# Performance work log

Hardware: AMD Instinct MI355X
Metric: run time of the kernel (lower is better)

The kernel has to match this reference:

```python
import jax, jax.numpy as jnp
import numpy as np

EMBEDDING = 1024
PARAMETERS = 4096

def setup_inputs() -> dict:
    key = jax.random.key(0)
    kx, kK, kV = jax.random.split(key, 3)
    x = jax.random.normal(kx, (4, 2048, EMBEDDING), dtype=jnp.float32)
    K = jax.random.normal(kK, (PARAMETERS, EMBEDDING), dtype=jnp.float32)
    V = jax.random.normal(kV, (PARAMETERS, EMBEDDING), dtype=jnp.float32)
    return {"x": x, "K": K, "V": V}

def reference(x, K, V):
    # scores: [b, s, p] = scale * x @ K.T
    scale = EMBEDDING ** (-0.5)
    scores = scale * jnp.einsum('bse,pe->bsp', x, K)
    attn = jax.nn.softmax(scores, axis=-1)
    # out: [b, s, e] = attn @ V
    return jnp.einsum('bsp,pe->bse', attn, V)
```

## Files before the change

### kernel.cpp

```cpp
#include <hip/hip_runtime.h>
#include <hip/hip_bf16.h>

typedef __bf16 bf16x8 __attribute__((ext_vector_type(8)));
typedef __bf16 bf16x4 __attribute__((ext_vector_type(4)));
typedef float floatx4 __attribute__((ext_vector_type(4)));

typedef __attribute__((address_space(1))) const void gas_void;
typedef __attribute__((address_space(3))) void las_void;

__device__ inline void async_load16(const void* g, void* l) {
  __builtin_amdgcn_global_load_lds((gas_void*)g, (las_void*)l, 16, 0, 0);
}

__global__ __launch_bounds__(256) void f32_to_bf16_kernel(const float* __restrict__ in,
                                                          __bf16* __restrict__ out, int n4) {
  int i = blockIdx.x * 256 + threadIdx.x;
  if (i < n4) {
    float4 v = ((const float4*)in)[i];
    bf16x4 o = {(__bf16)v.x, (__bf16)v.y, (__bf16)v.z, (__bf16)v.w};
    ((bf16x4*)out)[i] = o;
  }
}

__global__ __launch_bounds__(256) void transpose_convert_kernel(const float* __restrict__ V,
                                                                __bf16* __restrict__ Vt) {
  __shared__ float tile[64][65];
  const int bx = blockIdx.x;
  const int by = blockIdx.y;
  for (int i = threadIdx.x; i < 64 * 64; i += 256) {
    const int r = i >> 6, c = i & 63;
    tile[r][c] = V[(size_t)(bx * 64 + r) * 1024 + by * 64 + c];
  }
  __syncthreads();
  for (int i = threadIdx.x; i < 64 * 64; i += 256) {
    const int r = i >> 6, c = i & 63;
    Vt[(size_t)(by * 64 + r) * 4096 + bx * 64 + c] = (__bf16)tile[c][r];
  }
}

template <int MODE, int KS, int NS>
__global__ __launch_bounds__(256) void gemm_kernel(const __bf16* __restrict__ A,
                                                   const __bf16* __restrict__ B,
                                                   __bf16* __restrict__ Cb,
                                                   float* __restrict__ Cf,
                                                   float* __restrict__ lsum) {
  constexpr int BK = 32;
  __shared__ __bf16 As[128 * BK];
  __shared__ __bf16 Bs[128 * BK];
  const int t = threadIdx.x;
  const int lane = t & 63;
  const int w = t >> 6;
  const int wr = w >> 1, wc = w & 1;

  const int id = blockIdx.x;
  const int g = id & 7;
  const int s = id >> 3;
  const int mt = g * 8 + (s & 7);
  const int nt = s >> 3;
  const int m0 = mt * 128;
  const int n0 = nt * 128;

  const __bf16* Ab = A + (size_t)m0 * KS;
  const __bf16* Bb = B + (size_t)n0 * KS;

  floatx4 acc[4][4] = {};

  const int f0 = t * 16;
  const int row0 = f0 >> 6;
  const int ke0 = (f0 & 63) >> 1;
  const int f1 = 4096 + t * 16;
  const int row1 = f1 >> 6;
  const int ke1 = (f1 & 63) >> 1;

  for (int k0 = 0; k0 < KS; k0 += BK) {
    async_load16(Ab + (size_t)row0 * KS + k0 + ke0, (char*)As + f0);
    async_load16(Ab + (size_t)row1 * KS + k0 + ke1, (char*)As + f1);
    async_load16(Bb + (size_t)row0 * KS + k0 + ke0, (char*)Bs + f0);
    async_load16(Bb + (size_t)row1 * KS + k0 + ke1, (char*)Bs + f1);
    __builtin_amdgcn_s_waitcnt(0);
    __syncthreads();

    bf16x8 aF[4], bF[4];
    const int krd = (lane >> 4) * 16;
#pragma unroll
    for (int i = 0; i < 4; ++i) {
      const int mr = wr * 64 + i * 16 + (lane & 15);
      aF[i] = *(const bf16x8*)((const char*)As + mr * 64 + krd);
    }
#pragma unroll
    for (int j = 0; j < 4; ++j) {
      const int nr = wc * 64 + j * 16 + (lane & 15);
      bF[j] = *(const bf16x8*)((const char*)Bs + nr * 64 + krd);
    }
#pragma unroll
    for (int i = 0; i < 4; ++i)
#pragma unroll
      for (int j = 0; j < 4; ++j)
        acc[i][j] = __builtin_amdgcn_mfma_f32_16x16x32_bf16(aF[i], bF[j], acc[i][j], 0, 0, 0);
    __syncthreads();
  }

  const int cm = wr * 64 + ((lane >> 4) << 2);
  const int cn = wc * 64 + (lane & 15);
  if (MODE == 0) {
#pragma unroll
    for (int i = 0; i < 4; ++i)
#pragma unroll
      for (int r = 0; r < 4; ++r) {
        const int m = m0 + cm + i * 16 + r;
        float rs = 0.f;
#pragma unroll
        for (int j = 0; j < 4; ++j) {
          const float e = __expf(fminf(acc[i][j][r] * 0.03125f, 30.0f));
          rs += e;
          Cb[(size_t)m * NS + n0 + cn + j * 16] = (__bf16)e;
        }
        rs += __shfl_xor(rs, 1, 64);
        rs += __shfl_xor(rs, 2, 64);
        rs += __shfl_xor(rs, 4, 64);
        rs += __shfl_xor(rs, 8, 64);
        if ((lane & 15) == 0) atomicAdd(&lsum[m], rs);
      }
  } else {
#pragma unroll
    for (int i = 0; i < 4; ++i)
#pragma unroll
      for (int r = 0; r < 4; ++r) {
        const int m = m0 + cm + i * 16 + r;
        const float inv = 1.0f / lsum[m];
#pragma unroll
        for (int j = 0; j < 4; ++j)
          Cf[(size_t)m * NS + n0 + cn + j * 16] = acc[i][j][r] * inv;
      }
  }
}

extern "C" void kernel_launch(void* const* d_in, const int* in_sizes, int n_in,
                              void* d_out, int out_size, void* d_ws, size_t ws_size,
                              hipStream_t stream) {
  const float* x = (const float*)d_in[0];
  const float* K = (const float*)d_in[1];
  const float* V = (const float*)d_in[2];
  float* out = (float*)d_out;

  char* ws = (char*)d_ws;
  __bf16* xb = (__bf16*)ws;
  __bf16* Kb = (__bf16*)(ws + (16u << 20));
  __bf16* Vt = (__bf16*)(ws + (24u << 20));
  __bf16* P  = (__bf16*)(ws + (32u << 20));
  float*  l  = (float*)(ws + (96u << 20));

  f32_to_bf16_kernel<<<8192, 256, 0, stream>>>(x, xb, 8192 * 1024 / 4);
  f32_to_bf16_kernel<<<4096, 256, 0, stream>>>(K, Kb, 4096 * 1024 / 4);
  transpose_convert_kernel<<<dim3(64, 16), 256, 0, stream>>>(V, Vt);
  hipMemsetAsync(l, 0, 8192 * sizeof(float), stream);
  gemm_kernel<0, 1024, 4096><<<2048, 256, 0, stream>>>(xb, Kb, P, nullptr, l);
  gemm_kernel<1, 4096, 1024><<<512, 256, 0, stream>>>(P, Vt, nullptr, out, l);
}
```

Before: 282.5 us.

## Fuse preprocessing kernels and double GEMM K-tile with XOR-swizzled LDS layout

Result: faster. 267.7 us (-5.2%).

```diff
diff --git a/kernel.cpp b/kernel.cpp
--- a/kernel.cpp
+++ b/kernel.cpp
@@ -12,29 +12,46 @@
   __builtin_amdgcn_global_load_lds((gas_void*)g, (las_void*)l, 16, 0, 0);
 }
 
-__global__ __launch_bounds__(256) void f32_to_bf16_kernel(const float* __restrict__ in,
-                                                          __bf16* __restrict__ out, int n4) {
-  int i = blockIdx.x * 256 + threadIdx.x;
-  if (i < n4) {
-    float4 v = ((const float4*)in)[i];
-    bf16x4 o = {(__bf16)v.x, (__bf16)v.y, (__bf16)v.z, (__bf16)v.w};
-    ((bf16x4*)out)[i] = o;
-  }
-}
-
-__global__ __launch_bounds__(256) void transpose_convert_kernel(const float* __restrict__ V,
-                                                                __bf16* __restrict__ Vt) {
-  __shared__ float tile[64][65];
-  const int bx = blockIdx.x;
-  const int by = blockIdx.y;
-  for (int i = threadIdx.x; i < 64 * 64; i += 256) {
-    const int r = i >> 6, c = i & 63;
-    tile[r][c] = V[(size_t)(bx * 64 + r) * 1024 + by * 64 + c];
-  }
-  __syncthreads();
-  for (int i = threadIdx.x; i < 64 * 64; i += 256) {
-    const int r = i >> 6, c = i & 63;
-    Vt[(size_t)(by * 64 + r) * 4096 + bx * 64 + c] = (__bf16)tile[c][r];
+__global__ __launch_bounds__(256) void preprocess_kernel(
+    const float* __restrict__ x, const float* __restrict__ Kp,
+    const float* __restrict__ V, __bf16* __restrict__ xb,
+    __bf16* __restrict__ Kb, __bf16* __restrict__ Vt,
+    float* __restrict__ lsum) {
+  const int b = blockIdx.x;
+  const int t = threadIdx.x;
+  if (b < 2048) {
+#pragma unroll
+    for (int k = 0; k < 4; ++k) {
+      const int i = b * 1024 + k * 256 + t;
+      float4 v = ((const float4*)x)[i];
+      bf16x4 o = {(__bf16)v.x, (__bf16)v.y, (__bf16)v.z, (__bf16)v.w};
+      ((bf16x4*)xb)[i] = o;
+    }
+  } else if (b < 3072) {
+#pragma unroll
+    for (int k = 0; k < 4; ++k) {
+      const int i = (b - 2048) * 1024 + k * 256 + t;
+      float4 v = ((const float4*)Kp)[i];
+      bf16x4 o = {(__bf16)v.x, (__bf16)v.y, (__bf16)v.z, (__bf16)v.w};
+      ((bf16x4*)Kb)[i] = o;
+    }
+  } else if (b < 4096) {
+    __shared__ float tile[64][65];
+    const int bb = b - 3072;
+    const int bx = bb & 63, by = bb >> 6;
+    for (int i = t; i < 64 * 64; i += 256) {
+      const int r = i >> 6, c = i & 63;
+      tile[r][c] = V[(size_t)(bx * 64 + r) * 1024 + by * 64 + c];
+    }
+    __syncthreads();
+    for (int i = t; i < 64 * 64; i += 256) {
+      const int r = i >> 6, c = i & 63;
+      Vt[(size_t)(by * 64 + r) * 4096 + bx * 64 + c] = (__bf16)tile[c][r];
+    }
+  } else {
+#pragma unroll
+    for (int k = 0; k < 8; ++k)
+      ((floatx4*)lsum)[k * 256 + t] = floatx4{0.f, 0.f, 0.f, 0.f};
   }
 }
 
@@ -44,7 +61,7 @@
                                                    __bf16* __restrict__ Cb,
                                                    float* __restrict__ Cf,
                                                    float* __restrict__ lsum) {
-  constexpr int BK = 32;
+  constexpr int BK = 64;
   __shared__ __bf16 As[128 * BK];
   __shared__ __bf16 Bs[128 * BK];
   const int t = threadIdx.x;
@@ -65,32 +82,41 @@
 
   floatx4 acc[4][4] = {};
 
-  const int f0 = t * 16;
-  const int row0 = f0 >> 6;
-  const int ke0 = (f0 & 63) >> 1;
-  const int f1 = 4096 + t * 16;
-  const int row1 = f1 >> 6;
-  const int ke1 = (f1 & 63) >> 1;
+  const int mA = t >> 3;
+  const int qs = (t & 7) ^ (mA & 7);
+  const __bf16* aP = Ab + (size_t)mA * KS + qs * 8;
+  const __bf16* bP = Bb + (size_t)mA * KS + qs * 8;
+  char* dA = (char*)As + t * 16;
+  char* dB = (char*)Bs + t * 16;
+
+  const int rl = lane & 15;
+  const int qq = lane >> 4;
+  const int fo = rl * 128 + ((qq ^ (rl & 7)) << 4);
 
   for (int k0 = 0; k0 < KS; k0 += BK) {
-    async_load16(Ab + (size_t)row0 * KS + k0 + ke0, (char*)As + f0);
-    async_load16(Ab + (size_t)row1 * KS + k0 + ke1, (char*)As + f1);
-    async_load16(Bb + (size_t)row0 * KS + k0 + ke0, (char*)Bs + f0);
-    async_load16(Bb + (size_t)row1 * KS + k0 + ke1, (char*)Bs + f1);
+#pragma unroll
+    for (int r = 0; r < 4; ++r) {
+      async_load16(aP + (size_t)r * 32 * KS + k0, dA + r * 4096);
+      async_load16(bP + (size_t)r * 32 * KS + k0, dB + r * 4096);
+    }
     __builtin_amdgcn_s_waitcnt(0);
     __syncthreads();
 
     bf16x8 aF[4], bF[4];
-    const int krd = (lane >> 4) * 16;
 #pragma unroll
     for (int i = 0; i < 4; ++i) {
-      const int mr = wr * 64 + i * 16 + (lane & 15);
-      aF[i] = *(const bf16x8*)((const char*)As + mr * 64 + krd);
+      aF[i] = *(const bf16x8*)((const char*)As + wr * 8192 + i * 2048 + fo);
+      bF[i] = *(const bf16x8*)((const char*)Bs + wc * 8192 + i * 2048 + fo);
     }
 #pragma unroll
-    for (int j = 0; j < 4; ++j) {
-      const int nr = wc * 64 + j * 16 + (lane & 15);
-      bF[j] = *(const bf16x8*)((const char*)Bs + nr * 64 + krd);
+    for (int i = 0; i < 4; ++i)
+#pragma unroll
+      for (int j = 0; j < 4; ++j)
+        acc[i][j] = __builtin_amdgcn_mfma_f32_16x16x32_bf16(aF[i], bF[j], acc[i][j], 0, 0, 0);
+#pragma unroll
+    for (int i = 0; i < 4; ++i) {
+      aF[i] = *(const bf16x8*)((const char*)As + wr * 8192 + i * 2048 + (fo ^ 64));
+      bF[i] = *(const bf16x8*)((const char*)Bs + wc * 8192 + i * 2048 + (fo ^ 64));
     }
 #pragma unroll
     for (int i = 0; i < 4; ++i)
@@ -150,10 +176,7 @@
   __bf16* P  = (__bf16*)(ws + (32u << 20));
   float*  l  = (float*)(ws + (96u << 20));
 
-  f32_to_bf16_kernel<<<8192, 256, 0, stream>>>(x, xb, 8192 * 1024 / 4);
-  f32_to_bf16_kernel<<<4096, 256, 0, stream>>>(K, Kb, 4096 * 1024 / 4);
-  transpose_convert_kernel<<<dim3(64, 16), 256, 0, stream>>>(V, Vt);
-  hipMemsetAsync(l, 0, 8192 * sizeof(float), stream);
+  preprocess_kernel<<<4097, 256, 0, stream>>>(x, K, V, xb, Kb, Vt, l);
   gemm_kernel<0, 1024, 4096><<<2048, 256, 0, stream>>>(xb, Kb, P, nullptr, l);
   gemm_kernel<1, 4096, 1024><<<512, 256, 0, stream>>>(P, Vt, nullptr, out, l);
 }
```
